# Performance work log

Hardware: AMD Instinct MI355X
Metric: run time of the kernel (lower is better)

## Reference

```python
import jax, jax.numpy as jnp
import numpy as np

EMBED_DIM = 1280
NUM_HEADS = 20
HEAD_DIM = EMBED_DIM // NUM_HEADS  # 64
TGT_LEN = 2048
BSZ = 2
SCALING = HEAD_DIM ** -0.5


def setup_inputs() -> dict:
    key = jax.random.key(0)
    ks = jax.random.split(key, 6)
    s = EMBED_DIM ** -0.5
    query = jax.random.normal(ks[0], (TGT_LEN, BSZ, EMBED_DIM), dtype=jnp.float32)
    Wq = jax.random.normal(ks[1], (EMBED_DIM, EMBED_DIM), dtype=jnp.float32) * s
    Wk = jax.random.normal(ks[2], (EMBED_DIM, EMBED_DIM), dtype=jnp.float32) * s
    Wv = jax.random.normal(ks[3], (EMBED_DIM, EMBED_DIM), dtype=jnp.float32) * s
    Wo = jax.random.normal(ks[4], (EMBED_DIM, EMBED_DIM), dtype=jnp.float32) * s
    bq = jnp.zeros((EMBED_DIM,), jnp.float32)
    bk = jnp.zeros((EMBED_DIM,), jnp.float32)
    bv = jnp.zeros((EMBED_DIM,), jnp.float32)
    bo = jnp.zeros((EMBED_DIM,), jnp.float32)
    # key_padding_mask: (bsz, src_len), True = padded; pad last 256 keys of batch 1
    kpm = np.zeros((BSZ, TGT_LEN), dtype=bool)
    kpm[1, -256:] = True
    key_padding_mask = jnp.asarray(kpm)
    return {"query": query, "key_padding_mask": key_padding_mask,
            "Wq": Wq, "bq": bq, "Wk": Wk, "bk": bk,
            "Wv": Wv, "bv": bv, "Wo": Wo, "bo": bo}


def _mha(query, key_padding_mask, Wq, bq, Wk, bk, Wv, bv, Wo, bo):
    T, B, E = query.shape
    H, D = NUM_HEADS, HEAD_DIM
    q = (query @ Wq + bq) * SCALING            # [T, B, E]
    k = query @ Wk + bk
    v = query @ Wv + bv
    # reshape to [B*H, T, D] as in the TF code
    q = q.reshape(T, B * H, D).transpose(1, 0, 2)
    k = k.reshape(T, B * H, D).transpose(1, 0, 2)
    v = v.reshape(T, B * H, D).transpose(1, 0, 2)
    attn_weights = jnp.einsum('bqd,bkd->bqk', q, k)   # [B*H, T, T]
    # key padding mask: (B, src_len), 1s excluded -> -inf
    aw = attn_weights.reshape(B, H, T, T)
    aw = jnp.where(key_padding_mask[:, None, None, :], -jnp.inf, aw)
    attn_weights_float = jax.nn.softmax(aw.astype(jnp.float32).reshape(B * H, T, T), axis=-1)
    attn_probs = attn_weights_float.astype(v.dtype)  # dropout rate 0.0 -> identity
    attn = jnp.einsum('bqk,bkd->bqd', attn_probs, v)  # [B*H, T, D]
    attn = attn.transpose(1, 0, 2).reshape(T, B, E)
    attn = attn @ Wo + bo
    # need_weights=True (default), need_head_weights=False -> mean over heads
    avg_weights = attn_weights_float.reshape(B, H, T, T).transpose(1, 0, 2, 3).mean(axis=0)
    return attn, avg_weights


def reference(query, key_padding_mask, Wq, bq, Wk, bk, Wv, bv, Wo, bo):
    return _mha(query, key_padding_mask, Wq, bq, Wk, bk, Wv, bv, Wo, bo)
```

## Files before the change

### kernel.cpp

```cpp
#include <hip/hip_runtime.h>

#define T_LEN 2048
#define BSZ   2
#define EMB   1280
#define NH    20
#define HD    64
#define NBH   (BSZ*NH)
#define NR    (T_LEN*BSZ)
#define QSCALE (0.125f * 1.4426950408889634f)

typedef short bf16x8 __attribute__((ext_vector_type(8)));
typedef short bf16x4 __attribute__((ext_vector_type(4)));
typedef float f32x4  __attribute__((ext_vector_type(4)));

__device__ inline short f2bf(float f) {
    union { float f; unsigned u; } v; v.f = f;
    unsigned u = v.u + 0x7FFF + ((v.u >> 16) & 1);
    return (short)(u >> 16);
}

__global__ __launch_bounds__(256) void k_cvt_x(
    const float* __restrict__ X, short* __restrict__ Xb)
{
    size_t i0 = ((size_t)blockIdx.x*256 + threadIdx.x) * 8;
    float4 a = *(const float4*)(X + i0);
    float4 b = *(const float4*)(X + i0 + 4);
    bf16x8 r = { f2bf(a.x), f2bf(a.y), f2bf(a.z), f2bf(a.w),
                 f2bf(b.x), f2bf(b.y), f2bf(b.z), f2bf(b.w) };
    *(bf16x8*)(Xb + i0) = r;
}

__global__ __launch_bounds__(256) void k_cvt_wt(
    const float* __restrict__ Wq, const float* __restrict__ Wk,
    const float* __restrict__ Wv, const float* __restrict__ Wo,
    short* __restrict__ Wqt, short* __restrict__ Wkt,
    short* __restrict__ Wvt, short* __restrict__ Wot)
{
    const int z = blockIdx.z;
    const float* __restrict__ W = (z==0)?Wq:(z==1)?Wk:(z==2)?Wv:Wo;
    short* __restrict__ Wt      = (z==0)?Wqt:(z==1)?Wkt:(z==2)?Wvt:Wot;

    const int k0 = blockIdx.y * 32;
    const int n0 = blockIdx.x * 32;
    const int t  = threadIdx.x;

    __shared__ float Ls[32][33];
    {
        int row = t >> 3, col = (t & 7) * 4;
        *(float4*)&Ls[row][col] = *(const float4*)(W + (size_t)(k0+row)*EMB + n0 + col);
    }
    __syncthreads();
    {
        int n = t >> 3, k4 = (t & 7) * 4;
        bf16x4 r = { f2bf(Ls[k4+0][n]), f2bf(Ls[k4+1][n]),
                     f2bf(Ls[k4+2][n]), f2bf(Ls[k4+3][n]) };
        *(bf16x4*)(Wt + (size_t)(n0+n)*EMB + k0 + k4) = r;
    }
}

__global__ __launch_bounds__(256) void k_gemm_qkv(
    const short* __restrict__ Xb,
    const short* __restrict__ Wqt, const short* __restrict__ Wkt, const short* __restrict__ Wvt,
    const float* __restrict__ bq, const float* __restrict__ bk, const float* __restrict__ bv,
    short* __restrict__ Qb, short* __restrict__ Kb, short* __restrict__ Vt)
{
    const int which = blockIdx.z;
    const short* __restrict__ Wt   = (which==0) ? Wqt : (which==1) ? Wkt : Wvt;
    const float* __restrict__ bias = (which==0) ? bq  : (which==1) ? bk  : bv;
    const float scale = (which==0) ? QSCALE : 1.0f;

    const int bm = blockIdx.y * 128;
    const int bn = blockIdx.x * 128;
    const int t    = threadIdx.x;
    const int wave = t >> 6, lane = t & 63;
    const int l16  = lane & 15, quad = lane >> 4;
    const int wm   = (wave >> 1) * 64, wn = (wave & 1) * 64;

    __shared__ short As[128][72];
    __shared__ short Bs[128][72];

    f32x4 acc[4][4] = {};

    for (int kt = 0; kt < EMB; kt += 64) {
        __syncthreads();
        const short* Ag = Xb + (size_t)bm*EMB + kt;
        const short* Bg = Wt + (size_t)bn*EMB + kt;
        #pragma unroll
        for (int c = 0; c < 4; ++c) {
            int idx = c*256 + t;
            int row = idx >> 3, col8 = (idx & 7) * 8;
            *(bf16x8*)&As[row][col8] = *(const bf16x8*)(Ag + (size_t)row*EMB + col8);
            *(bf16x8*)&Bs[row][col8] = *(const bf16x8*)(Bg + (size_t)row*EMB + col8);
        }
        __syncthreads();
        #pragma unroll
        for (int ks = 0; ks < 64; ks += 32) {
            bf16x8 af[4], bfr[4];
            #pragma unroll
            for (int mi=0;mi<4;++mi) af[mi]  = *(const bf16x8*)&As[wm + mi*16 + l16][ks + quad*8];
            #pragma unroll
            for (int ni=0;ni<4;++ni) bfr[ni] = *(const bf16x8*)&Bs[wn + ni*16 + l16][ks + quad*8];
            #pragma unroll
            for (int mi=0;mi<4;++mi)
                #pragma unroll
                for (int ni=0;ni<4;++ni)
                    acc[mi][ni] = __builtin_amdgcn_mfma_f32_16x16x32_bf16(af[mi], bfr[ni], acc[mi][ni], 0,0,0);
        }
    }

    #pragma unroll
    for (int ni=0;ni<4;++ni) {
        int c = bn + wn + ni*16 + l16;
        float bval = bias[c];
        int h = c >> 6, d = c & 63;
        #pragma unroll
        for (int mi=0;mi<4;++mi) {
            #pragma unroll
            for (int j=0;j<4;++j) {
                int r = bm + wm + mi*16 + quad*4 + j;
                int tt = r >> 1, bb = r & 1;
                float val = (acc[mi][ni][j] + bval) * scale;
                if (which == 2)
                    Vt[((size_t)(bb*NH+h)*HD + d)*T_LEN + tt] = f2bf(val);
                else {
                    short* dst = (which==0) ? Qb : Kb;
                    dst[((size_t)(bb*NH+h)*T_LEN + tt)*HD + d] = f2bf(val);
                }
            }
        }
    }
}

__global__ __launch_bounds__(256) void k_pv(
    const short* __restrict__ Qb, const short* __restrict__ Kb, const short* __restrict__ Vt,
    const int* __restrict__ kpm,
    float* __restrict__ Linv,
    short* __restrict__ AttnMidb)
{
    const int qt = blockIdx.x;
    const int bh = blockIdx.y;
    const int b  = bh / NH, h = bh % NH;
    const int t    = threadIdx.x;
    const int w    = t >> 6;
    const int lane = t & 63;
    const int l16  = lane & 15;
    const int quad = lane >> 4;
    const int q0   = qt*128 + w*32;

    __shared__ short Ks[64][72];
    __shared__ short Vts[64][72];
    __shared__ short Ps[4][32][40];
    __shared__ float Mf[64];
    __shared__ float Lsh[128];

    bf16x8 qf[2][2];
    #pragma unroll
    for (int mi=0;mi<2;++mi)
        #pragma unroll
        for (int ch=0;ch<2;++ch)
            qf[mi][ch] = *(const bf16x8*)(Qb + ((size_t)bh*T_LEN + q0 + mi*16 + l16)*HD + ch*32 + quad*8);

    f32x4 o[2][4] = {};
    float l[2] = {0.f, 0.f};

    for (int kt = 0; kt < T_LEN; kt += 64) {
        __syncthreads();
        #pragma unroll
        for (int c2 = 0; c2 < 2; ++c2) {
            int idx = c2*256 + t;
            int row = idx >> 3, col8 = (idx & 7)*8;
            *(bf16x8*)&Ks[row][col8]  = *(const bf16x8*)(Kb + ((size_t)bh*T_LEN + kt + row)*HD + col8);
            *(bf16x8*)&Vts[row][col8] = *(const bf16x8*)(Vt + ((size_t)bh*HD + row)*T_LEN + kt + col8);
        }
        if (t < 64) Mf[t] = kpm[b*T_LEN + kt + t] ? 0.f : 1.f;
        __syncthreads();

        f32x4 s[4][2] = {};
        #pragma unroll
        for (int ch = 0; ch < 2; ++ch) {
            bf16x8 ka[4];
            #pragma unroll
            for (int mb=0;mb<4;++mb) ka[mb] = *(const bf16x8*)&Ks[mb*16 + l16][ch*32 + quad*8];
            #pragma unroll
            for (int mb=0;mb<4;++mb)
                #pragma unroll
                for (int mi=0;mi<2;++mi)
                    s[mb][mi] = __builtin_amdgcn_mfma_f32_16x16x32_bf16(ka[mb], qf[mi][ch], s[mb][mi], 0,0,0);
        }

        #pragma unroll
        for (int c = 0; c < 2; ++c) {
            #pragma unroll
            for (int mb2 = 0; mb2 < 2; ++mb2) {
                const int mb = c*2 + mb2;
                float4 mf = *(const float4*)&Mf[mb*16 + quad*4];
                #pragma unroll
                for (int mi = 0; mi < 2; ++mi) {
                    float p0 = __builtin_amdgcn_exp2f(s[mb][mi][0]) * mf.x;
                    float p1 = __builtin_amdgcn_exp2f(s[mb][mi][1]) * mf.y;
                    float p2 = __builtin_amdgcn_exp2f(s[mb][mi][2]) * mf.z;
                    float p3 = __builtin_amdgcn_exp2f(s[mb][mi][3]) * mf.w;
                    l[mi] += (p0 + p1) + (p2 + p3);
                    unsigned d0 = ((unsigned)(unsigned short)f2bf(p1) << 16) | (unsigned short)f2bf(p0);
                    unsigned d1 = ((unsigned)(unsigned short)f2bf(p3) << 16) | (unsigned short)f2bf(p2);
                    uint2 dd; dd.x = d0; dd.y = d1;
                    *(uint2*)&Ps[w][mi*16 + l16][mb2*16 + quad*4] = dd;
                }
            }
            #pragma unroll
            for (int mi=0;mi<2;++mi) {
                bf16x8 pa = *(const bf16x8*)&Ps[w][mi*16 + l16][quad*8];
                #pragma unroll
                for (int nb=0;nb<4;++nb) {
                    bf16x8 vb = *(const bf16x8*)&Vts[nb*16 + l16][c*32 + quad*8];
                    o[mi][nb] = __builtin_amdgcn_mfma_f32_16x16x32_bf16(pa, vb, o[mi][nb], 0,0,0);
                }
            }
        }
    }

    #pragma unroll
    for (int mi=0;mi<2;++mi) {
        l[mi] += __shfl_xor(l[mi], 16);
        l[mi] += __shfl_xor(l[mi], 32);
        float linv = 1.0f / l[mi];
        if (quad == 0) {
            Linv[(size_t)bh*T_LEN + q0 + mi*16 + l16] = linv;
            Lsh[w*32 + mi*16 + l16] = linv;
        }
    }
    #pragma unroll
    for (int mi=0;mi<2;++mi) {
        float4 li = *(const float4*)&Lsh[w*32 + mi*16 + quad*4];
        float lr[4] = {li.x, li.y, li.z, li.w};
        #pragma unroll
        for (int r=0;r<4;++r) {
            int q = q0 + mi*16 + quad*4 + r;
            size_t base = ((size_t)q*BSZ + b)*EMB + h*HD;
            #pragma unroll
            for (int nb=0;nb<4;++nb)
                AttnMidb[base + nb*16 + l16] = f2bf(o[mi][nb][r] * lr[r]);
        }
    }
}

__global__ __launch_bounds__(256) void k_meanw(
    const short* __restrict__ Qb, const short* __restrict__ Kb,
    const int* __restrict__ kpm,
    const float* __restrict__ Linv,
    float* __restrict__ avg)
{
    const int kt = blockIdx.x;
    const int qt = blockIdx.y;
    const int b  = blockIdx.z;
    const int t    = threadIdx.x;
    const int wave = t >> 6, lane = t & 63;
    const int l16  = lane & 15, quad = lane >> 4;

    __shared__ short Qs[64][72];
    __shared__ short Ks[64][72];
    __shared__ float Lish[64];
    __shared__ int   msk[64];

    if (t < 64) msk[t] = kpm[b*T_LEN + kt*64 + t];

    f32x4 acc[4] = {};
    const int qrow_in = wave*16 + quad*4;

    for (int h = 0; h < NH; ++h) {
        const int bh = b*NH + h;
        __syncthreads();
        {
            const short* Qg = Qb + ((size_t)bh*T_LEN + qt*64)*HD;
            const short* Kg = Kb + ((size_t)bh*T_LEN + kt*64)*HD;
            #pragma unroll
            for (int c = 0; c < 2; ++c) {
                int idx = c*256 + t;
                int row = idx >> 3, col8 = (idx & 7) * 8;
                *(bf16x8*)&Qs[row][col8] = *(const bf16x8*)(Qg + (size_t)row*HD + col8);
                *(bf16x8*)&Ks[row][col8] = *(const bf16x8*)(Kg + (size_t)row*HD + col8);
            }
        }
        if (t < 64) Lish[t] = Linv[(size_t)bh*T_LEN + qt*64 + t];
        __syncthreads();

        bf16x8 aq0 = *(const bf16x8*)&Qs[wave*16 + l16][quad*8];
        bf16x8 aq1 = *(const bf16x8*)&Qs[wave*16 + l16][32 + quad*8];

        float lv[4];
        #pragma unroll
        for (int r = 0; r < 4; ++r)
            lv[r] = Lish[qrow_in + r] * (1.0f/NH);

        #pragma unroll
        for (int nb = 0; nb < 4; ++nb) {
            bf16x8 bk0 = *(const bf16x8*)&Ks[nb*16 + l16][quad*8];
            bf16x8 bk1 = *(const bf16x8*)&Ks[nb*16 + l16][32 + quad*8];
            f32x4 s = {};
            s = __builtin_amdgcn_mfma_f32_16x16x32_bf16(aq0, bk0, s, 0,0,0);
            s = __builtin_amdgcn_mfma_f32_16x16x32_bf16(aq1, bk1, s, 0,0,0);
            const bool mk = msk[nb*16 + l16] != 0;
            #pragma unroll
            for (int r = 0; r < 4; ++r)
                acc[nb][r] += mk ? 0.f : __builtin_amdgcn_exp2f(s[r]) * lv[r];
        }
    }

    #pragma unroll
    for (int r = 0; r < 4; ++r) {
        int q = qt*64 + qrow_in + r;
        size_t base = ((size_t)b*T_LEN + q) * T_LEN + (size_t)kt*64;
        #pragma unroll
        for (int nb = 0; nb < 4; ++nb)
            avg[base + nb*16 + l16] = acc[nb][r];
    }
}

__global__ __launch_bounds__(256) void k_gemm_out(
    const short* __restrict__ Ab, const short* __restrict__ Wot,
    const float* __restrict__ bo, float* __restrict__ out)
{
    const int bm = blockIdx.y * 128;
    const int bn = blockIdx.x * 128;
    const int t    = threadIdx.x;
    const int wave = t >> 6, lane = t & 63;
    const int l16  = lane & 15, quad = lane >> 4;
    const int wm   = (wave >> 1) * 64, wn = (wave & 1) * 64;

    __shared__ short As[128][72];
    __shared__ short Bs[128][72];

    f32x4 acc[4][4] = {};

    for (int kt = 0; kt < EMB; kt += 64) {
        __syncthreads();
        const short* Ag = Ab  + (size_t)bm*EMB + kt;
        const short* Bg = Wot + (size_t)bn*EMB + kt;
        #pragma unroll
        for (int c = 0; c < 4; ++c) {
            int idx = c*256 + t;
            int row = idx >> 3, col8 = (idx & 7) * 8;
            *(bf16x8*)&As[row][col8] = *(const bf16x8*)(Ag + (size_t)row*EMB + col8);
            *(bf16x8*)&Bs[row][col8] = *(const bf16x8*)(Bg + (size_t)row*EMB + col8);
        }
        __syncthreads();
        #pragma unroll
        for (int ks = 0; ks < 64; ks += 32) {
            bf16x8 af[4], bfr[4];
            #pragma unroll
            for (int mi=0;mi<4;++mi) af[mi]  = *(const bf16x8*)&As[wm + mi*16 + l16][ks + quad*8];
            #pragma unroll
            for (int ni=0;ni<4;++ni) bfr[ni] = *(const bf16x8*)&Bs[wn + ni*16 + l16][ks + quad*8];
            #pragma unroll
            for (int mi=0;mi<4;++mi)
                #pragma unroll
                for (int ni=0;ni<4;++ni)
                    acc[mi][ni] = __builtin_amdgcn_mfma_f32_16x16x32_bf16(af[mi], bfr[ni], acc[mi][ni], 0,0,0);
        }
    }

    #pragma unroll
    for (int ni=0;ni<4;++ni) {
        int c = bn + wn + ni*16 + l16;
        float bval = bo[c];
        #pragma unroll
        for (int mi=0;mi<4;++mi) {
            #pragma unroll
            for (int j=0;j<4;++j) {
                int r = bm + wm + mi*16 + quad*4 + j;
                out[(size_t)r*EMB + c] = acc[mi][ni][j] + bval;
            }
        }
    }
}

extern "C" void kernel_launch(void* const* d_in, const int* in_sizes, int n_in,
                              void* d_out, int out_size, void* d_ws, size_t ws_size,
                              hipStream_t stream) {
    const float* X   = (const float*)d_in[0];
    const int*   kpm = (const int*)  d_in[1];
    const float* Wq  = (const float*)d_in[2];
    const float* bq  = (const float*)d_in[3];
    const float* Wk  = (const float*)d_in[4];
    const float* bk  = (const float*)d_in[5];
    const float* Wv  = (const float*)d_in[6];
    const float* bv  = (const float*)d_in[7];
    const float* Wo  = (const float*)d_in[8];
    const float* bo  = (const float*)d_in[9];

    float* out = (float*)d_out;
    float* ws  = (float*)d_ws;

    const size_t QKV = (size_t)NBH * T_LEN * HD;
    float* Linv = ws;
    short* Xb   = (short*)(Linv + (size_t)NBH * T_LEN);
    short* Wqt  = Xb  + (size_t)NR * EMB;
    short* Wkt  = Wqt + (size_t)EMB * EMB;
    short* Wvt  = Wkt + (size_t)EMB * EMB;
    short* Wot  = Wvt + (size_t)EMB * EMB;
    short* Qb   = Wot + (size_t)EMB * EMB;
    short* Kb   = Qb  + QKV;
    short* Vt   = Kb  + QKV;
    short* Amid = Vt  + QKV;

    float* attn_out = out;
    float* avg      = out + (size_t)T_LEN * BSZ * EMB;

    k_cvt_x   <<<dim3((NR*EMB)/(256*8)), 256, 0, stream>>>(X, Xb);
    k_cvt_wt  <<<dim3(EMB/32, EMB/32, 4), 256, 0, stream>>>(Wq, Wk, Wv, Wo, Wqt, Wkt, Wvt, Wot);
    k_gemm_qkv<<<dim3(EMB/128, NR/128, 3), 256, 0, stream>>>(Xb, Wqt, Wkt, Wvt, bq, bk, bv, Qb, Kb, Vt);
    k_pv      <<<dim3(T_LEN/128, NBH),   256, 0, stream>>>(Qb, Kb, Vt, kpm, Linv, Amid);
    k_meanw   <<<dim3(T_LEN/64, T_LEN/64, BSZ), 256, 0, stream>>>(Qb, Kb, kpm, Linv, avg);
    k_gemm_out<<<dim3(EMB/128, NR/128),  256, 0, stream>>>(Amid, Wot, bo, attn_out);
}
```

Before: 358.2 us.

## Double-buffer K/V tiles and keep P in registers in PV kernel

Adds double-buffered shared-memory K/V/mask tiles with a register prefetch of the next tile, so only one barrier per iteration is needed and global loads overlap compute. Probabilities are packed to bf16 with the hardware cvt_pk instruction and fed straight from registers into the PV MFMA. The V fragments are read in a permuted k-order that matches the register layout of P, which removes the Ps shared-memory round trip. The cost is higher LDS use and register pressure, and the permuted ordering must stay consistent between P and V.

```diff
diff --git a/kernel.cpp b/kernel.cpp
--- a/kernel.cpp
+++ b/kernel.cpp
@@ -17,6 +17,12 @@
     union { float f; unsigned u; } v; v.f = f;
     unsigned u = v.u + 0x7FFF + ((v.u >> 16) & 1);
     return (short)(u >> 16);
+}
+
+__device__ inline unsigned cvt_pk_bf16(float lo, float hi) {
+    unsigned r;
+    asm("v_cvt_pk_bf16_f32 %0, %1, %2" : "=v"(r) : "v"(lo), "v"(hi));
+    return r;
 }
 
 __global__ __launch_bounds__(256) void k_cvt_x(
@@ -147,10 +153,9 @@
     const int quad = lane >> 4;
     const int q0   = qt*128 + w*32;
 
-    __shared__ short Ks[64][72];
-    __shared__ short Vts[64][72];
-    __shared__ short Ps[4][32][40];
-    __shared__ float Mf[64];
+    __shared__ short Ks[2][64][72];
+    __shared__ short Vts[2][64][72];
+    __shared__ float MfL[2][64];
     __shared__ float Lsh[128];
 
     bf16x8 qf[2][2];
@@ -160,27 +165,42 @@
         for (int ch=0;ch<2;++ch)
             qf[mi][ch] = *(const bf16x8*)(Qb + ((size_t)bh*T_LEN + q0 + mi*16 + l16)*HD + ch*32 + quad*8);
 
+    const int row0 = t >> 3, col8 = (t & 7) * 8;
+    const short* Kgb = Kb + (size_t)bh*T_LEN*HD;
+    const short* Vgb = Vt + (size_t)bh*HD*T_LEN;
+
+    *(bf16x8*)&Ks[0][row0][col8]      = *(const bf16x8*)(Kgb + (size_t)row0*HD + col8);
+    *(bf16x8*)&Ks[0][row0+32][col8]   = *(const bf16x8*)(Kgb + (size_t)(row0+32)*HD + col8);
+    *(bf16x8*)&Vts[0][row0][col8]     = *(const bf16x8*)(Vgb + (size_t)row0*T_LEN + col8);
+    *(bf16x8*)&Vts[0][row0+32][col8]  = *(const bf16x8*)(Vgb + (size_t)(row0+32)*T_LEN + col8);
+    if (t < 64) MfL[0][t] = kpm[b*T_LEN + t] ? 0.f : 1.f;
+    __syncthreads();
+
     f32x4 o[2][4] = {};
     float l[2] = {0.f, 0.f};
+    int cur = 0;
 
     for (int kt = 0; kt < T_LEN; kt += 64) {
-        __syncthreads();
-        #pragma unroll
-        for (int c2 = 0; c2 < 2; ++c2) {
-            int idx = c2*256 + t;
-            int row = idx >> 3, col8 = (idx & 7)*8;
-            *(bf16x8*)&Ks[row][col8]  = *(const bf16x8*)(Kb + ((size_t)bh*T_LEN + kt + row)*HD + col8);
-            *(bf16x8*)&Vts[row][col8] = *(const bf16x8*)(Vt + ((size_t)bh*HD + row)*T_LEN + kt + col8);
-        }
-        if (t < 64) Mf[t] = kpm[b*T_LEN + kt + t] ? 0.f : 1.f;
-        __syncthreads();
+        const int ktn = kt + 64;
+        const bool has_next = ktn < T_LEN;
+        const int nxt = cur ^ 1;
+
+        bf16x8 kr0, kr1, vr0, vr1;
+        float mfn = 0.f;
+        if (has_next) {
+            kr0 = *(const bf16x8*)(Kgb + (size_t)(ktn + row0)*HD + col8);
+            kr1 = *(const bf16x8*)(Kgb + (size_t)(ktn + row0 + 32)*HD + col8);
+            vr0 = *(const bf16x8*)(Vgb + (size_t)row0*T_LEN + ktn + col8);
+            vr1 = *(const bf16x8*)(Vgb + (size_t)(row0+32)*T_LEN + ktn + col8);
+            if (t < 64) mfn = kpm[b*T_LEN + ktn + t] ? 0.f : 1.f;
+        }
 
         f32x4 s[4][2] = {};
         #pragma unroll
         for (int ch = 0; ch < 2; ++ch) {
             bf16x8 ka[4];
             #pragma unroll
-            for (int mb=0;mb<4;++mb) ka[mb] = *(const bf16x8*)&Ks[mb*16 + l16][ch*32 + quad*8];
+            for (int mb=0;mb<4;++mb) ka[mb] = *(const bf16x8*)&Ks[cur][mb*16 + l16][ch*32 + quad*8];
             #pragma unroll
             for (int mb=0;mb<4;++mb)
                 #pragma unroll
@@ -188,12 +208,13 @@
                     s[mb][mi] = __builtin_amdgcn_mfma_f32_16x16x32_bf16(ka[mb], qf[mi][ch], s[mb][mi], 0,0,0);
         }
 
+        unsigned pu[2][2][4];
         #pragma unroll
         for (int c = 0; c < 2; ++c) {
             #pragma unroll
             for (int mb2 = 0; mb2 < 2; ++mb2) {
                 const int mb = c*2 + mb2;
-                float4 mf = *(const float4*)&Mf[mb*16 + quad*4];
+                float4 mf = *(const float4*)&MfL[cur][mb*16 + quad*4];
                 #pragma unroll
                 for (int mi = 0; mi < 2; ++mi) {
                     float p0 = __builtin_amdgcn_exp2f(s[mb][mi][0]) * mf.x;
@@ -201,22 +222,42 @@
                     float p2 = __builtin_amdgcn_exp2f(s[mb][mi][2]) * mf.z;
                     float p3 = __builtin_amdgcn_exp2f(s[mb][mi][3]) * mf.w;
                     l[mi] += (p0 + p1) + (p2 + p3);
-                    unsigned d0 = ((unsigned)(unsigned short)f2bf(p1) << 16) | (unsigned short)f2bf(p0);
-                    unsigned d1 = ((unsigned)(unsigned short)f2bf(p3) << 16) | (unsigned short)f2bf(p2);
-                    uint2 dd; dd.x = d0; dd.y = d1;
-                    *(uint2*)&Ps[w][mi*16 + l16][mb2*16 + quad*4] = dd;
+                    pu[c][mi][mb2*2+0] = cvt_pk_bf16(p0, p1);
+                    pu[c][mi][mb2*2+1] = cvt_pk_bf16(p2, p3);
                 }
             }
+        }
+
+        if (has_next) {
+            *(bf16x8*)&Ks[nxt][row0][col8]      = kr0;
+            *(bf16x8*)&Ks[nxt][row0+32][col8]   = kr1;
+            *(bf16x8*)&Vts[nxt][row0][col8]     = vr0;
+            *(bf16x8*)&Vts[nxt][row0+32][col8]  = vr1;
+            if (t < 64) MfL[nxt][t] = mfn;
+        }
+
+        #pragma unroll
+        for (int c = 0; c < 2; ++c) {
+            bf16x8 vv[4];
+            #pragma unroll
+            for (int nb=0;nb<4;++nb) {
+                bf16x4 va = *(const bf16x4*)&Vts[cur][nb*16 + l16][c*32 + quad*4];
+                bf16x4 vb = *(const bf16x4*)&Vts[cur][nb*16 + l16][c*32 + 16 + quad*4];
+                vv[nb] = (bf16x8){va[0],va[1],va[2],va[3], vb[0],vb[1],vb[2],vb[3]};
+            }
             #pragma unroll
             for (int mi=0;mi<2;++mi) {
-                bf16x8 pa = *(const bf16x8*)&Ps[w][mi*16 + l16][quad*8];
+                union { unsigned u[4]; bf16x8 v; } pa;
+                pa.u[0]=pu[c][mi][0]; pa.u[1]=pu[c][mi][1];
+                pa.u[2]=pu[c][mi][2]; pa.u[3]=pu[c][mi][3];
                 #pragma unroll
-                for (int nb=0;nb<4;++nb) {
-                    bf16x8 vb = *(const bf16x8*)&Vts[nb*16 + l16][c*32 + quad*8];
-                    o[mi][nb] = __builtin_amdgcn_mfma_f32_16x16x32_bf16(pa, vb, o[mi][nb], 0,0,0);
-                }
-            }
-        }
+                for (int nb=0;nb<4;++nb)
+                    o[mi][nb] = __builtin_amdgcn_mfma_f32_16x16x32_bf16(pa.v, vv[nb], o[mi][nb], 0,0,0);
+            }
+        }
+
+        __syncthreads();
+        cur = nxt;
     }
 
     #pragma unroll
```

After: 357.0 us. About the same (-0.3%).
